# Optimization experiments

Hardware: AMD Instinct MI355X
Metric: run time of the kernel (lower is better)

The kernel has to match this reference:

```python
import jax, jax.numpy as jnp
import numpy as np

SIGMA = (2.0, 5.0, 10.0, 20.0, 40.0, 60.0)  # RBF bandwidths from __init__
MAX_SEG = 16  # static upper bound on number of class segments (== n classes in gt)


def setup_inputs() -> dict:
    key = jax.random.key(0)
    k1, k2, k3 = jax.random.split(key, 3)
    B, C, H, W = 1, 128, 64, 64
    predict = jax.random.normal(k1, (B, C, H, W), dtype=jnp.float32)
    target = jax.random.normal(k2, (B, C, H, W), dtype=jnp.float32)
    # sorted_randint -> contiguous variable-size class segments, as the torch loop assumes
    gt = jnp.sort(jax.random.randint(k3, (B * H * W,), 0, MAX_SEG)).reshape(B, H, W)
    ignore_mask = jnp.ones((B, H, W), dtype=bool)  # all pixels visible
    return {"predict": predict, "target": target, "gt": gt, "ignore_mask": ignore_mask}


def _sqdist(a, b):
    # ||a_i - b_j||^2 ; prob_mat in the original is -0.5 * this
    aa = jnp.sum(a * a, axis=1)
    bb = jnp.sum(b * b, axis=1)
    return aa[:, None] + bb[None, :] - 2.0 * (a @ b.T)


def reference(predict, target, gt, ignore_mask):
    d = predict.shape[1]
    # [B,C,H,W] -> [V,C]; ignore_mask is all True so visible set == all pixels
    pf = predict.transpose(0, 2, 3, 1).reshape(-1, d)
    tf = target.transpose(0, 2, 3, 1).reshape(-1, d)
    cls = gt.reshape(-1)

    # segment id = index of contiguous class run (what the Python boundary loop computes)
    boundary = (cls[1:] != cls[:-1]).astype(jnp.int32)
    seg = jnp.concatenate([jnp.zeros((1,), jnp.int32), jnp.cumsum(boundary)])
    counts = jax.ops.segment_sum(jnp.ones(seg.shape, predict.dtype), seg, num_segments=MAX_SEG)

    # pairwise squared distances within/between predict and target (shared across segments)
    Dpp = _sqdist(pf, pf)
    Dtt = _sqdist(tf, tf)
    Dpt = _sqdist(pf, tf)

    # Per segment with M=N=n: ww is +1/(2n^2) on pp/tt blocks, -1/(2n^2) on cross blocks,
    # and sum over the tp block equals sum over the pt block. So
    # loss_s = (1/(2 n^2)) * sum_bw sum_{i,j in s} (Kpp + Ktt - 2 Kpt)_{ij}
    C = jnp.zeros_like(Dpp)
    for bw in SIGMA:
        inv = -0.5 / bw  # K = exp(prob/bw) = exp(-||x_i-x_j||^2 / (2 bw))
        C = C + jnp.exp(inv * Dpp) + jnp.exp(inv * Dtt) - 2.0 * jnp.exp(inv * Dpt)

    same = seg[:, None] == seg[None, :]
    C = jnp.where(same, C, 0.0)
    seg_tot = jax.ops.segment_sum(jnp.sum(C, axis=1), seg, num_segments=MAX_SEG)

    denom = jnp.maximum(2.0 * counts * counts, 1.0)
    loss_s = jnp.where(counts > 0, seg_tot / denom, 0.0)
    pos = loss_s > 0
    loss_s = jnp.where(pos, jnp.sqrt(jnp.where(pos, loss_s, 1.0)), 0.0)  # sqrt(loss) if >0 else 0

    class_count = jnp.sum(counts > 0).astype(predict.dtype)
    return jnp.sum(loss_s) / class_count
```

## Files before the change

kernel.cpp:

```cpp
#include <hip/hip_runtime.h>
#include <math.h>

#define NCLS 16
#define TS   64
#define CH   32
#define PAD  36
#define NB   512
#define PIXB 16

typedef float vfloat4 __attribute__((ext_vector_type(4), aligned(4)));

struct Ctl {
    int   counts[NCLS];
    int   starts[NCLS + 1];
    int   tpc[NCLS];
    int   pairBase[NCLS + 1];
    float classSum[NCLS];
};

__global__ __launch_bounds__(256) void prep_kernel(
    const float* __restrict__ P, const float* __restrict__ T,
    const int* __restrict__ gt, int V, int D,
    Ctl* __restrict__ ctl,
    float* __restrict__ normP, float* __restrict__ normT,
    int nbNorm) {
    const int b = blockIdx.x;
    const int t = threadIdx.x;
    if (b < nbNorm) {
        __shared__ float pP[16][PIXB + 1], pT[16][PIXB + 1];
        const int pix = t & (PIXB - 1);
        const int dl  = t >> 4;
        const int v   = b * PIXB + pix;
        float np = 0.f, nt = 0.f;
        if (v < V) {
            #pragma unroll 4
            for (int d = dl; d < D; d += 16) {
                float x = P[(long)d * V + v]; np += x * x;
                float y = T[(long)d * V + v]; nt += y * y;
            }
        }
        pP[dl][pix] = np; pT[dl][pix] = nt;
        __syncthreads();
        if (t < PIXB && b * PIXB + t < V) {
            float sp = 0.f, st = 0.f;
            #pragma unroll
            for (int k = 0; k < 16; ++k) { sp += pP[k][t]; st += pT[k][t]; }
            normP[b * PIXB + t] = sp;
            normT[b * PIXB + t] = st;
        }
    } else {
        if (t < NCLS) {
            int lo = 0, hi = V;
            while (lo < hi) {
                int mid = (lo + hi) >> 1;
                if (gt[mid] < t) lo = mid + 1; else hi = mid;
            }
            ctl->starts[t] = lo;
            ctl->classSum[t] = 0.0f;
        }
        if (t == 0) ctl->starts[NCLS] = V;
        __syncthreads();
        if (t == 0) {
            int pb = 0;
            for (int c = 0; c < NCLS; ++c) {
                int n = ctl->starts[c + 1] - ctl->starts[c];
                ctl->counts[c] = n;
                int tp = (n + TS - 1) / TS;
                ctl->tpc[c] = tp;
                ctl->pairBase[c] = pb;
                pb += tp * tp;
            }
            ctl->pairBase[NCLS] = pb;
        }
    }
}

__global__ __launch_bounds__(256) void mmd_kernel(
    const float* __restrict__ P, const float* __restrict__ T,
    int V, int D, const Ctl* __restrict__ ctl,
    const float* __restrict__ normP, const float* __restrict__ normT,
    float* __restrict__ classSum)
{
    __shared__ float sPr[TS][PAD], sTr[TS][PAD];
    __shared__ float sPc[TS][PAD], sTc[TS][PAD];
    __shared__ float wsum[4];

    const int t  = threadIdx.x;
    const int tx = t & 15;
    const int ty = t >> 4;
    const int sd = t >> 3;
    const int qb = t & 7;
    const int W  = ctl->pairBase[NCLS];

    const float invs[6] = {-0.25f, -0.1f, -0.05f, -0.025f, -0.0125f, -1.0f/120.0f};

    for (int w = blockIdx.x; w < W; w += gridDim.x) {
        int c = 0;
        while (ctl->pairBase[c + 1] <= w) ++c;
        const int local = w - ctl->pairBase[c];
        const int tp    = ctl->tpc[c];
        const int ti    = local / tp;
        const int tj    = local - ti * tp;
        const int n     = ctl->counts[c];
        const int start = ctl->starts[c];
        const int i0    = ti * TS;
        const int j0    = tj * TS;

        const int r0 = i0 + 4 * qb;
        const int r1 = i0 + 4 * qb + 32;
        const int c0 = j0 + 4 * qb;
        const int c1 = j0 + 4 * qb + 32;

        vfloat4 vPr0, vPr1, vTr0, vTr1, vPc0, vPc1, vTc0, vTc1;

        auto load_quad = [&](long off, int rb, vfloat4& vP, vfloat4& vT) {
            if (rb + 3 < n) {
                vP = *(const vfloat4*)&P[off + start + rb];
                vT = *(const vfloat4*)&T[off + start + rb];
            } else {
                int a0 = start + min(rb,     n - 1);
                int a1 = start + min(rb + 1, n - 1);
                int a2 = start + min(rb + 2, n - 1);
                int a3 = start + min(rb + 3, n - 1);
                vP = (vfloat4){P[off + a0], P[off + a1], P[off + a2], P[off + a3]};
                vT = (vfloat4){T[off + a0], T[off + a1], T[off + a2], T[off + a3]};
            }
        };
        auto issue_loads = [&](int dcc) {
            const long off = (long)(dcc + sd) * (long)V;
            load_quad(off, r0, vPr0, vTr0);
            load_quad(off, r1, vPr1, vTr1);
            load_quad(off, c0, vPc0, vTc0);
            load_quad(off, c1, vPc1, vTc1);
        };

        float dpp[4][4], dtt[4][4], dpt[4][4];
        #pragma unroll
        for (int a = 0; a < 4; ++a)
            #pragma unroll
            for (int b = 0; b < 4; ++b) { dpp[a][b] = 0.f; dtt[a][b] = 0.f; dpt[a][b] = 0.f; }

        issue_loads(0);

        #pragma unroll 1
        for (int dc = 0; dc < D; dc += CH) {
            __syncthreads();
            #pragma unroll
            for (int k = 0; k < 4; ++k) {
                sPr[4*qb +      k][sd] = vPr0[k];
                sPr[4*qb + 32 + k][sd] = vPr1[k];
                sTr[4*qb +      k][sd] = vTr0[k];
                sTr[4*qb + 32 + k][sd] = vTr1[k];
                sPc[4*qb +      k][sd] = vPc0[k];
                sPc[4*qb + 32 + k][sd] = vPc1[k];
                sTc[4*qb +      k][sd] = vTc0[k];
                sTc[4*qb + 32 + k][sd] = vTc1[k];
            }
            __syncthreads();
            if (dc + CH < D)
                issue_loads(dc + CH);

            #pragma unroll 1
            for (int dg = 0; dg < CH; dg += 4) {
                float4 rP[4], rT[4], cP[4], cT[4];
                #pragma unroll
                for (int a = 0; a < 4; ++a) {
                    rP[a] = *(const float4*)&sPr[ty + 16*a][dg];
                    rT[a] = *(const float4*)&sTr[ty + 16*a][dg];
                    cP[a] = *(const float4*)&sPc[tx + 16*a][dg];
                    cT[a] = *(const float4*)&sTc[tx + 16*a][dg];
                }
                #pragma unroll
                for (int a = 0; a < 4; ++a)
                    #pragma unroll
                    for (int b = 0; b < 4; ++b)
                        dpp[a][b] += rP[a].x*cP[b].x + rP[a].y*cP[b].y
                                   + rP[a].z*cP[b].z + rP[a].w*cP[b].w;
                #pragma unroll
                for (int a = 0; a < 4; ++a)
                    #pragma unroll
                    for (int b = 0; b < 4; ++b)
                        dpt[a][b] += rP[a].x*cT[b].x + rP[a].y*cT[b].y
                                   + rP[a].z*cT[b].z + rP[a].w*cT[b].w;
                #pragma unroll
                for (int a = 0; a < 4; ++a)
                    #pragma unroll
                    for (int b = 0; b < 4; ++b)
                        dtt[a][b] += rT[a].x*cT[b].x + rT[a].y*cT[b].y
                                   + rT[a].z*cT[b].z + rT[a].w*cT[b].w;
            }
        }

        float total = 0.0f;
        #pragma unroll
        for (int a = 0; a < 4; ++a) {
            const int ii = i0 + ty + 16*a;
            if (ii < n) {
                const float nPi = normP[start + ii];
                const float nTi = normT[start + ii];
                #pragma unroll
                for (int b = 0; b < 4; ++b) {
                    const int jj = j0 + tx + 16*b;
                    if (jj < n) {
                        const float nPj = normP[start + jj];
                        const float nTj = normT[start + jj];
                        float Dpp = nPi + nPj - 2.0f * dpp[a][b];
                        float Dtt = nTi + nTj - 2.0f * dtt[a][b];
                        float Dpt = nPi + nTj - 2.0f * dpt[a][b];
                        #pragma unroll
                        for (int s = 0; s < 6; ++s) {
                            total += __expf(invs[s] * Dpp)
                                   + __expf(invs[s] * Dtt)
                                   - 2.0f * __expf(invs[s] * Dpt);
                        }
                    }
                }
            }
        }

        #pragma unroll
        for (int off = 32; off > 0; off >>= 1)
            total += __shfl_down(total, off, 64);
        if ((t & 63) == 0) wsum[t >> 6] = total;
        __syncthreads();
        if (t == 0)
            atomicAdd(&classSum[c], wsum[0] + wsum[1] + wsum[2] + wsum[3]);
    }
}

__global__ void finalize_kernel(const int* __restrict__ counts,
                                const float* __restrict__ classSum,
                                float* __restrict__ out) {
    if (threadIdx.x == 0) {
        float loss = 0.0f;
        int k = 0;
        for (int c = 0; c < NCLS; ++c) {
            int n = counts[c];
            if (n > 0) {
                ++k;
                float fn    = (float)n;
                float denom = fmaxf(2.0f * fn * fn, 1.0f);
                float l     = classSum[c] / denom;
                if (l > 0.0f) loss += sqrtf(l);
            }
        }
        out[0] = (k > 0) ? (loss / (float)k) : 0.0f;
    }
}

extern "C" void kernel_launch(void* const* d_in, const int* in_sizes, int n_in,
                              void* d_out, int out_size, void* d_ws, size_t ws_size,
                              hipStream_t stream) {
    const float* predict = (const float*)d_in[0];
    const float* target  = (const float*)d_in[1];
    const int*   gt      = (const int*)d_in[2];

    const int V = in_sizes[2];
    const int D = in_sizes[0] / V;

    Ctl* ctl = (Ctl*)d_ws;
    size_t normOff = (sizeof(Ctl) + 15) & ~(size_t)15;
    float* normP = (float*)((char*)d_ws + normOff);
    float* normT = normP + V;
    float* classSum = (float*)((char*)d_ws + offsetof(Ctl, classSum));

    int nbNorm = (V + PIXB - 1) / PIXB;
    prep_kernel<<<nbNorm + 1, 256, 0, stream>>>(predict, target, gt, V, D,
                                                ctl, normP, normT, nbNorm);

    mmd_kernel<<<NB, 256, 0, stream>>>(predict, target, V, D, ctl,
                                       normP, normT, classSum);

    finalize_kernel<<<1, 64, 0, stream>>>(ctl->counts, classSum, (float*)d_out);
}
```

Baseline: 105.0 us.

## Exploit kernel symmetry by computing only upper-triangular tile pairs per class

Enumerates only upper-triangular tile pairs (ti<=tj) within each class segment and doubles off-diagonal contributions. The aim is to cut the number of tile-pair work items roughly in half. For the symmetry to hold, each tile must now compute both the pt and tp cross terms, so it does a fourth 4x4 dot-product accumulator and 8 exps per element instead of 6. Diagonal tiles skip loading the column operands and reuse the row shared-memory tiles. The serial while-loop that decodes the triangular index adds some scalar overhead.

```diff
diff --git a/kernel.cpp b/kernel.cpp
--- a/kernel.cpp
+++ b/kernel.cpp
@@ -68,7 +68,7 @@
                 int tp = (n + TS - 1) / TS;
                 ctl->tpc[c] = tp;
                 ctl->pairBase[c] = pb;
-                pb += tp * tp;
+                pb += tp * (tp + 1) / 2;
             }
             ctl->pairBase[NCLS] = pb;
         }
@@ -97,14 +97,16 @@
     for (int w = blockIdx.x; w < W; w += gridDim.x) {
         int c = 0;
         while (ctl->pairBase[c + 1] <= w) ++c;
-        const int local = w - ctl->pairBase[c];
-        const int tp    = ctl->tpc[c];
-        const int ti    = local / tp;
-        const int tj    = local - ti * tp;
-        const int n     = ctl->counts[c];
-        const int start = ctl->starts[c];
-        const int i0    = ti * TS;
-        const int j0    = tj * TS;
+        const int tp = ctl->tpc[c];
+        int rem = w - ctl->pairBase[c];
+        int ti = 0;
+        while (rem >= tp - ti) { rem -= (tp - ti); ++ti; }
+        const int tj     = ti + rem;
+        const bool diag  = (ti == tj);
+        const int n      = ctl->counts[c];
+        const int start  = ctl->starts[c];
+        const int i0     = ti * TS;
+        const int j0     = tj * TS;
 
         const int r0 = i0 + 4 * qb;
         const int r1 = i0 + 4 * qb + 32;
@@ -130,15 +132,21 @@
             const long off = (long)(dcc + sd) * (long)V;
             load_quad(off, r0, vPr0, vTr0);
             load_quad(off, r1, vPr1, vTr1);
-            load_quad(off, c0, vPc0, vTc0);
-            load_quad(off, c1, vPc1, vTc1);
+            if (!diag) {
+                load_quad(off, c0, vPc0, vTc0);
+                load_quad(off, c1, vPc1, vTc1);
+            }
         };
 
-        float dpp[4][4], dtt[4][4], dpt[4][4];
+        const float (*sCp)[PAD] = diag ? sPr : sPc;
+        const float (*sCt)[PAD] = diag ? sTr : sTc;
+
+        float dpp[4][4], dtt[4][4], dpt[4][4], dtp[4][4];
         #pragma unroll
         for (int a = 0; a < 4; ++a)
             #pragma unroll
-            for (int b = 0; b < 4; ++b) { dpp[a][b] = 0.f; dtt[a][b] = 0.f; dpt[a][b] = 0.f; }
+            for (int b = 0; b < 4; ++b)
+                { dpp[a][b] = 0.f; dtt[a][b] = 0.f; dpt[a][b] = 0.f; dtp[a][b] = 0.f; }
 
         issue_loads(0);
 
@@ -151,10 +159,15 @@
                 sPr[4*qb + 32 + k][sd] = vPr1[k];
                 sTr[4*qb +      k][sd] = vTr0[k];
                 sTr[4*qb + 32 + k][sd] = vTr1[k];
-                sPc[4*qb +      k][sd] = vPc0[k];
-                sPc[4*qb + 32 + k][sd] = vPc1[k];
-                sTc[4*qb +      k][sd] = vTc0[k];
-                sTc[4*qb + 32 + k][sd] = vTc1[k];
+            }
+            if (!diag) {
+                #pragma unroll
+                for (int k = 0; k < 4; ++k) {
+                    sPc[4*qb +      k][sd] = vPc0[k];
+                    sPc[4*qb + 32 + k][sd] = vPc1[k];
+                    sTc[4*qb +      k][sd] = vTc0[k];
+                    sTc[4*qb + 32 + k][sd] = vTc1[k];
+                }
             }
             __syncthreads();
             if (dc + CH < D)
@@ -167,8 +180,8 @@
                 for (int a = 0; a < 4; ++a) {
                     rP[a] = *(const float4*)&sPr[ty + 16*a][dg];
                     rT[a] = *(const float4*)&sTr[ty + 16*a][dg];
-                    cP[a] = *(const float4*)&sPc[tx + 16*a][dg];
-                    cT[a] = *(const float4*)&sTc[tx + 16*a][dg];
+                    cP[a] = *(const float4*)&sCp[tx + 16*a][dg];
+                    cT[a] = *(const float4*)&sCt[tx + 16*a][dg];
                 }
                 #pragma unroll
                 for (int a = 0; a < 4; ++a)
@@ -188,9 +201,16 @@
                     for (int b = 0; b < 4; ++b)
                         dtt[a][b] += rT[a].x*cT[b].x + rT[a].y*cT[b].y
                                    + rT[a].z*cT[b].z + rT[a].w*cT[b].w;
-            }
-        }
-
+                #pragma unroll
+                for (int a = 0; a < 4; ++a)
+                    #pragma unroll
+                    for (int b = 0; b < 4; ++b)
+                        dtp[a][b] += rT[a].x*cP[b].x + rT[a].y*cP[b].y
+                                   + rT[a].z*cP[b].z + rT[a].w*cP[b].w;
+            }
+        }
+
+        const float f = diag ? 1.0f : 2.0f;
         float total = 0.0f;
         #pragma unroll
         for (int a = 0; a < 4; ++a) {
@@ -207,12 +227,14 @@
                         float Dpp = nPi + nPj - 2.0f * dpp[a][b];
                         float Dtt = nTi + nTj - 2.0f * dtt[a][b];
                         float Dpt = nPi + nTj - 2.0f * dpt[a][b];
+                        float Dtp = nTi + nPj - 2.0f * dtp[a][b];
+                        float s6 = 0.0f;
                         #pragma unroll
                         for (int s = 0; s < 6; ++s) {
-                            total += __expf(invs[s] * Dpp)
-                                   + __expf(invs[s] * Dtt)
-                                   - 2.0f * __expf(invs[s] * Dpt);
+                            s6 += __expf(invs[s] * Dpp) + __expf(invs[s] * Dtt)
+                                - __expf(invs[s] * Dpt) - __expf(invs[s] * Dtp);
                         }
+                        total += f * s6;
                     }
                 }
             }
```

Measured after the change: 100.5 us. -4.3%, faster.
